# Kernel tuning notes

Measured on AMD Instinct MI355X. Metric: run time of the kernel, lower is better.

The kernel has to match this reference:

```python
import jax, jax.numpy as jnp
import numpy as np

B, L, D = 8, 1024, 768
H, W, Dd = 16, 16, 4          # token grid, H*W*Dd == L
N, R, K = 16, 48, 4           # d_state, dt_rank, d_conv
EPS = 1e-5


def _physical_pos_embed(batch_params, has_velocity):
    # physical coords [B, L, 3]: (distance, angle, velocity/time)
    h_idx = jnp.arange(H, dtype=jnp.float32)[None, :, None, None]
    w_idx = jnp.arange(W, dtype=jnp.float32)[None, None, :, None]
    d_idx = jnp.arange(Dd, dtype=jnp.float32)[None, None, None, :]
    rres = batch_params[:, 0][:, None, None, None]
    ares = batch_params[:, 1][:, None, None, None]
    vres = batch_params[:, 2][:, None, None, None]
    zero = jnp.zeros((1, H, W, Dd), jnp.float32)
    dist = h_idx * rres + zero
    ang = (w_idx - W / 2) * ares + zero
    vel = jnp.where(has_velocity[:, None, None, None],
                    (d_idx - Dd / 2) * vres, d_idx * vres) + zero
    coords = jnp.stack([dist, ang, vel], axis=-1).reshape(B, L, 3)
    mx = coords.max(axis=1, keepdims=True)
    mn = coords.min(axis=1, keepdims=True)
    rng = mx - mn
    rng = jnp.where(rng > 0, rng, jnp.ones_like(rng))
    coords = (coords - mn) / rng
    # sincos embed: D/3 = 256 dims per coord (even -> pure sin/cos)
    fdim = D // 3
    omega = jnp.arange(fdim // 2, dtype=jnp.float32) / (fdim / 2.0)
    omega = 1.0 / (10000.0 ** omega)                      # [128]
    out = jnp.einsum('blc,f->blcf', coords, omega)        # [B,L,3,128]
    emb = jnp.concatenate([jnp.sin(out), jnp.cos(out)], axis=-1)  # [B,L,3,256]
    return emb.reshape(B, L, D)


def _rmsnorm(x, w):
    return x * jax.lax.rsqrt(jnp.mean(x * x, axis=-1, keepdims=True) + EPS) * w


def _mamba(h, in_proj_w, in_proj_b, conv_w, conv_b, x_proj_w,
           dt_proj_w, dt_proj_b, A_log, D_param, out_proj_w, out_proj_b):
    xz = h @ in_proj_w.T + in_proj_b                      # [B,L,2D]
    x_in, z = xz[..., :D], xz[..., D:]
    # causal depthwise conv1d, kernel K
    xp = jnp.pad(x_in, ((0, 0), (K - 1, 0), (0, 0)))
    x_conv = sum(xp[:, k:k + L, :] * conv_w[:, 0, k] for k in range(K))
    x_conv = jax.nn.silu(x_conv + conv_b)
    x_dbl = x_conv @ x_proj_w.T                           # [B,L,R+2N]
    dt, Bm, Cm = x_dbl[..., :R], x_dbl[..., R:R + N], x_dbl[..., R + N:]
    dt = jax.nn.softplus(dt @ dt_proj_w.T + dt_proj_b)    # [B,L,D]
    A = -jnp.exp(A_log)                                   # [D,N]
    dA = jnp.exp(dt[..., None] * A)                       # [B,L,D,N]
    dBx = dt[..., None] * Bm[:, :, None, :] * x_conv[..., None]

    def step(hst, inp):
        dA_t, dBx_t, C_t = inp
        hst = dA_t * hst + dBx_t                          # [B,D,N]
        y_t = jnp.einsum('bdn,bn->bd', hst, C_t)
        return hst, y_t

    h0 = jnp.zeros((B, D, N), x_in.dtype)
    _, ys = jax.lax.scan(step, h0, (dA.transpose(1, 0, 2, 3),
                                    dBx.transpose(1, 0, 2, 3),
                                    Cm.transpose(1, 0, 2)))
    y = ys.transpose(1, 0, 2) + D_param * x_conv          # [B,L,D]
    y = y * jax.nn.silu(z)
    return y @ out_proj_w.T + out_proj_b


def reference(x, batch_params, has_velocity, norm_w, in_proj_w, in_proj_b,
              conv_w, conv_b, x_proj_w, dt_proj_w, dt_proj_b, A_log,
              D_param, out_proj_w, out_proj_b):
    pos = _physical_pos_embed(batch_params, has_velocity)
    residual = x + pos                                    # ARBlock residual
    hidden = _rmsnorm(residual, norm_w)
    hidden = _mamba(hidden, in_proj_w, in_proj_b, conv_w, conv_b, x_proj_w,
                    dt_proj_w, dt_proj_b, A_log, D_param,
                    out_proj_w, out_proj_b)
    return hidden + residual


def setup_inputs():
    key = jax.random.key(0)
    ks = jax.random.split(key, 12)
    s = 0.02
    return {
        'x': jax.random.normal(ks[0], (B, L, D), jnp.float32),
        'batch_params': jax.random.uniform(ks[1], (B, 4), jnp.float32, 0.01, 1.0),
        'has_velocity': jax.random.randint(ks[2], (B,), 0, 2) > 0,
        'norm_w': jnp.ones((D,), jnp.float32),
        'in_proj_w': jax.random.normal(ks[3], (2 * D, D), jnp.float32) * s,
        'in_proj_b': jnp.zeros((2 * D,), jnp.float32),
        'conv_w': jax.random.normal(ks[4], (D, 1, K), jnp.float32) * 0.3,
        'conv_b': jnp.zeros((D,), jnp.float32),
        'x_proj_w': jax.random.normal(ks[5], (R + 2 * N, D), jnp.float32) * s,
        'dt_proj_w': jax.random.normal(ks[6], (D, R), jnp.float32) * s,
        'dt_proj_b': jax.random.normal(ks[7], (D,), jnp.float32) * 0.1,
        'A_log': jnp.log(jax.random.uniform(ks[8], (D, N), jnp.float32, 1.0, 16.0)),
        'D_param': jnp.ones((D,), jnp.float32),
        'out_proj_w': jax.random.normal(ks[9], (D, D), jnp.float32) * s,
        'out_proj_b': jnp.zeros((D,), jnp.float32),
    }
```

## Files before the change

kernel.cpp:

```cpp
#include <hip/hip_runtime.h>
#include <math.h>

#define BB 8
#define LL 1024
#define DD 768
#define NNs 16
#define RR 48

typedef __attribute__((ext_vector_type(8))) short bf16x8;
typedef __attribute__((ext_vector_type(4))) float f32x4;

__device__ __forceinline__ float silu_f(float v) { return v / (1.0f + __expf(-v)); }

__device__ __forceinline__ short f2bf(float f) {
    union { float f; unsigned u; } v; v.f = f;
    unsigned r = (v.u + 0x7fffu + ((v.u >> 16) & 1u)) >> 16;
    return (short)r;
}

__device__ __forceinline__ void async16(const void* g, void* l) {
    __builtin_amdgcn_global_load_lds((const __attribute__((address_space(1))) void*)g,
                                     (__attribute__((address_space(3))) void*)l,
                                     16, 0, 0);
}

__global__ __launch_bounds__(256) void k_cvt(const float* __restrict__ src,
                                             short* __restrict__ dst, int n4) {
    int i = blockIdx.x * 256 + threadIdx.x;
    if (i < n4) {
        float4 v = ((const float4*)src)[i];
        short4 o = { f2bf(v.x), f2bf(v.y), f2bf(v.z), f2bf(v.w) };
        ((short4*)dst)[i] = o;
    }
}

__global__ __launch_bounds__(256) void k_pos_rms(const float* __restrict__ x,
                                                 const float* __restrict__ norm_w,
                                                 float* __restrict__ res,
                                                 short* __restrict__ hidb) {
    int row = blockIdx.x;
    int l = row & (LL - 1);
    int d3 = l & 3;
    int w = (l >> 2) & 15;
    int h = l >> 6;
    float coord[3] = { h * (1.0f / 15.0f), w * (1.0f / 15.0f), d3 * (1.0f / 3.0f) };
    const float LOG1E4 = 9.210340371976184f;
    int t = threadIdx.x;
    float r[3];
    float s = 0.0f;
#pragma unroll
    for (int i = 0; i < 3; i++) {
        int j = t + i * 256;
        int c = j >> 8;
        int fp = j & 255;
        int f = fp & 127;
        float omega = __expf(-(f * (1.0f / 128.0f)) * LOG1E4);
        float arg = coord[c] * omega;
        float pv = (fp < 128) ? __sinf(arg) : __cosf(arg);
        float rv = x[(size_t)row * DD + j] + pv;
        r[i] = rv;
        s += rv * rv;
    }
#pragma unroll
    for (int off = 32; off; off >>= 1) s += __shfl_xor(s, off, 64);
    __shared__ float ls[4];
    if ((t & 63) == 0) ls[t >> 6] = s;
    __syncthreads();
    s = ls[0] + ls[1] + ls[2] + ls[3];
    float rs = rsqrtf(s * (1.0f / DD) + 1e-5f);
#pragma unroll
    for (int i = 0; i < 3; i++) {
        int j = t + i * 256;
        res[(size_t)row * DD + j] = r[i];
        hidb[(size_t)row * DD + j] = f2bf(r[i] * rs * norm_w[j]);
    }
}

template <int EPI, bool AF32>
__global__ __launch_bounds__(256) void gemm_mfma(const void* __restrict__ Ap,
                                                 const short* __restrict__ Bw,
                                                 int Kd,
                                                 const float* __restrict__ bias,
                                                 const float* __restrict__ resid,
                                                 float* __restrict__ C0,
                                                 float* __restrict__ C1) {
    __shared__ short As[4096];
    __shared__ short Bs[4096];
    int m0 = blockIdx.y * 128;
    int n0 = blockIdx.x * 128;
    int tid = threadIdx.x;
    int lane = tid & 63, wave = tid >> 6;
    int q = lane >> 4, r = lane & 15;
    int wm = wave >> 1, wn = wave & 1;

    const size_t Kb = (size_t)Kd * 2;
    const char* gB0 = (const char*)Bw + (size_t)(n0 + wave * 16 + r) * Kb + q * 16;
    const char* gB1 = gB0 + 64 * Kb;
    char* lB0 = (char*)Bs + wave * 1024;
    char* lB1 = lB0 + 4096;
    const char* gA0 = nullptr; const char* gA1 = nullptr;
    char* lA0 = nullptr; char* lA1 = nullptr;
    if (!AF32) {
        gA0 = (const char*)Ap + (size_t)(m0 + wave * 16 + r) * Kb + q * 16;
        gA1 = gA0 + 64 * Kb;
        lA0 = (char*)As + wave * 1024;
        lA1 = lA0 + 4096;
    }

    f32x4 acc[4][4] = {};

    for (int k0 = 0; k0 < Kd; k0 += 32) {
        if (AF32) {
            const float* Af = (const float*)Ap;
#pragma unroll
            for (int p = 0; p < 2; p++) {
                int m = m0 + (p * 4 + wave) * 16 + r;
                const float* src = Af + (size_t)m * Kd + k0 + q * 8;
                float4 v0 = *(const float4*)src;
                float4 v1 = *(const float4*)(src + 4);
                bf16x8 pk;
                pk[0] = f2bf(v0.x); pk[1] = f2bf(v0.y);
                pk[2] = f2bf(v0.z); pk[3] = f2bf(v0.w);
                pk[4] = f2bf(v1.x); pk[5] = f2bf(v1.y);
                pk[6] = f2bf(v1.z); pk[7] = f2bf(v1.w);
                *(bf16x8*)&As[p * 2048 + wave * 512 + lane * 8] = pk;
            }
        } else {
            async16(gA0, lA0); async16(gA1, lA1);
            gA0 += 64; gA1 += 64;
        }
        async16(gB0, lB0); async16(gB1, lB1);
        gB0 += 64; gB1 += 64;
        __syncthreads();
        bf16x8 af[4], bf[4];
#pragma unroll
        for (int a = 0; a < 4; a++)
            af[a] = *(const bf16x8*)&As[((wm * 4 + a) * 64 + q * 16 + r) * 8];
#pragma unroll
        for (int b = 0; b < 4; b++)
            bf[b] = *(const bf16x8*)&Bs[((wn * 4 + b) * 64 + q * 16 + r) * 8];
#pragma unroll
        for (int a = 0; a < 4; a++)
#pragma unroll
            for (int b = 0; b < 4; b++)
                acc[a][b] = __builtin_amdgcn_mfma_f32_16x16x32_bf16(
                    af[a], bf[b], acc[a][b], 0, 0, 0);
        __syncthreads();
    }

#pragma unroll
    for (int a = 0; a < 4; a++) {
        int mrow = m0 + (wm * 4 + a) * 16 + q * 4;
#pragma unroll
        for (int b = 0; b < 4; b++) {
            int ncol = n0 + (wn * 4 + b) * 16 + r;
            float bb = bias[ncol];
            if (EPI == 1) {
                float* dst = (ncol < DD) ? (C0 + (size_t)mrow * DD + ncol)
                                         : (C1 + (size_t)mrow * DD + (ncol - DD));
#pragma unroll
                for (int e = 0; e < 4; e++)
                    dst[(size_t)e * DD] = acc[a][b][e] + bb;
            } else {
#pragma unroll
                for (int e = 0; e < 4; e++) {
                    size_t idx = (size_t)(mrow + e) * DD + ncol;
                    C0[idx] = acc[a][b][e] + bb + resid[idx];
                }
            }
        }
    }
}

template <int MODE>
__global__ __launch_bounds__(256) void gemm_nt(const float* __restrict__ A, int lda,
                                               const float* __restrict__ Bw, int ldb,
                                               int N, int Kd,
                                               const float* __restrict__ bias,
                                               float* __restrict__ C0, int ldc) {
    __shared__ __align__(16) float As[16][68];
    __shared__ __align__(16) float Bs[16][68];
    int m0 = blockIdx.y * 64;
    int n0 = blockIdx.x * 64;
    int t = threadIdx.x;
    int tx = t & 15, ty = t >> 4;
    int ar = t >> 2;
    int ak = (t & 3) * 4;
    float acc[4][4] = {};
    for (int k0 = 0; k0 < Kd; k0 += 16) {
        float4 av = *(const float4*)(A + (size_t)(m0 + ar) * lda + k0 + ak);
        int brow = n0 + ar;
        if (brow >= N) brow = N - 1;
        float4 bv = *(const float4*)(Bw + (size_t)brow * ldb + k0 + ak);
        As[ak + 0][ar] = av.x; As[ak + 1][ar] = av.y;
        As[ak + 2][ar] = av.z; As[ak + 3][ar] = av.w;
        Bs[ak + 0][ar] = bv.x; Bs[ak + 1][ar] = bv.y;
        Bs[ak + 2][ar] = bv.z; Bs[ak + 3][ar] = bv.w;
        __syncthreads();
#pragma unroll
        for (int kk = 0; kk < 16; kk++) {
            float4 a4 = *(const float4*)&As[kk][ty * 4];
            float4 b4 = *(const float4*)&Bs[kk][tx * 4];
            float aa[4] = { a4.x, a4.y, a4.z, a4.w };
            float bb[4] = { b4.x, b4.y, b4.z, b4.w };
#pragma unroll
            for (int i = 0; i < 4; i++)
#pragma unroll
                for (int j = 0; j < 4; j++) acc[i][j] += aa[i] * bb[j];
        }
        __syncthreads();
    }
    if (MODE == 0) {
#pragma unroll
        for (int i = 0; i < 4; i++) {
            int m = m0 + ty * 4 + i;
#pragma unroll
            for (int j = 0; j < 4; j++) {
                int n = n0 + tx * 4 + j;
                if (n < N) C0[(size_t)m * ldc + n] = acc[i][j];
            }
        }
    } else {
        float4 bi = *(const float4*)(bias + n0 + tx * 4);
        float bl[4] = { bi.x, bi.y, bi.z, bi.w };
#pragma unroll
        for (int i = 0; i < 4; i++) {
            int m = m0 + ty * 4 + i;
            float v[4];
#pragma unroll
            for (int j = 0; j < 4; j++) {
                float u = acc[i][j] + bl[j];
                v[j] = (u > 20.0f) ? u : log1pf(__expf(u));
            }
            float4 o = { v[0], v[1], v[2], v[3] };
            *(float4*)(C0 + (size_t)m * DD + n0 + tx * 4) = o;
        }
    }
}

__global__ __launch_bounds__(256) void k_conv(const float* __restrict__ xin,
                                              const float* __restrict__ cw,
                                              const float* __restrict__ cb,
                                              float* __restrict__ xc) {
    size_t gid = (size_t)blockIdx.x * 256 + threadIdx.x;
    int d = (int)(gid % DD);
    int bt = (int)(gid / DD);
    int tt = bt & (LL - 1);
    float4 w = ((const float4*)cw)[d];
    const float* p = xin + (size_t)bt * DD + d;
    float acc = cb[d];
    if (tt >= 3) acc += p[-3 * DD] * w.x;
    if (tt >= 2) acc += p[-2 * DD] * w.y;
    if (tt >= 1) acc += p[-1 * DD] * w.z;
    acc += p[0] * w.w;
    xc[gid] = silu_f(acc);
}

__global__ __launch_bounds__(256) void k_scan(const float* __restrict__ dtf,
                                              const float* __restrict__ xc,
                                              const float* __restrict__ xdbl,
                                              const float* __restrict__ A_log,
                                              const float* __restrict__ Dp,
                                              float* __restrict__ zy) {
    __shared__ float Pl[32 * 8 * 16];
    __shared__ float Sl[32 * 8 * 16];
    int bid = blockIdx.x;
    int xcd = bid & 7;
    int v = bid >> 3;
    int dtile = xcd * 12 + (v % 12);
    int b = v / 12;
    int d0 = dtile * 8;
    int tid = threadIdx.x;
    int dl = tid & 7;
    int c = tid >> 3;
    int d = d0 + dl;

    float Ac[16];
    {
        const float4* al = (const float4*)(A_log + d * NNs);
#pragma unroll
        for (int i = 0; i < 4; i++) {
            float4 v4 = al[i];
            Ac[i * 4 + 0] = -__expf(v4.x); Ac[i * 4 + 1] = -__expf(v4.y);
            Ac[i * 4 + 2] = -__expf(v4.z); Ac[i * 4 + 3] = -__expf(v4.w);
        }
    }
    size_t rb = ((size_t)(b * LL + c * 32)) * DD + d;
    const float* dtp = dtf + rb;
    const float* xcp = xc + rb;
    float* zp = zy + rb;
    const float* xrow = xdbl + ((size_t)(b * LL + c * 32)) * 80 + RR;

    float P[16], S[16];
#pragma unroll
    for (int n = 0; n < 16; n++) { P[n] = 1.0f; S[n] = 0.0f; }
    for (int i = 0; i < 32; i++) {
        float dtv = dtp[(size_t)i * DD];
        float xcv = xcp[(size_t)i * DD];
        float dx = dtv * xcv;
        const float* Br = xrow + i * 80;
#pragma unroll
        for (int qq = 0; qq < 4; qq++) {
            float4 B4 = *(const float4*)(Br + qq * 4);
            float bl[4] = { B4.x, B4.y, B4.z, B4.w };
#pragma unroll
            for (int j = 0; j < 4; j++) {
                int n = qq * 4 + j;
                float e = __expf(dtv * Ac[n]);
                P[n] *= e;
                S[n] = e * S[n] + dx * bl[j];
            }
        }
    }
    {
        float* pw = &Pl[(c * 8 + dl) * 16];
        float* sw = &Sl[(c * 8 + dl) * 16];
#pragma unroll
        for (int qq = 0; qq < 4; qq++) {
            float4 pv = { P[qq * 4], P[qq * 4 + 1], P[qq * 4 + 2], P[qq * 4 + 3] };
            float4 sv = { S[qq * 4], S[qq * 4 + 1], S[qq * 4 + 2], S[qq * 4 + 3] };
            *(float4*)(pw + qq * 4) = pv;
            *(float4*)(sw + qq * 4) = sv;
        }
    }
    __syncthreads();
    if (tid < 128) {
        int d2 = tid >> 4, n2 = tid & 15;
        float hh = 0.0f;
#pragma unroll
        for (int cc = 0; cc < 32; cc++) {
            int idx = (cc * 8 + d2) * 16 + n2;
            float Pv = Pl[idx], Sv = Sl[idx];
            Pl[idx] = hh;
            hh = Pv * hh + Sv;
        }
    }
    __syncthreads();
    float h[16];
    {
        const float* hr = &Pl[(c * 8 + dl) * 16];
#pragma unroll
        for (int qq = 0; qq < 4; qq++) {
            float4 v4 = *(const float4*)(hr + qq * 4);
            h[qq * 4] = v4.x; h[qq * 4 + 1] = v4.y;
            h[qq * 4 + 2] = v4.z; h[qq * 4 + 3] = v4.w;
        }
    }
    float Dv = Dp[d];
    for (int i = 0; i < 32; i++) {
        float dtv = dtp[(size_t)i * DD];
        float xcv = xcp[(size_t)i * DD];
        float zv  = zp[(size_t)i * DD];
        float dx = dtv * xcv;
        float y = Dv * xcv;
        const float* Br = xrow + i * 80;
#pragma unroll
        for (int qq = 0; qq < 4; qq++) {
            float4 B4 = *(const float4*)(Br + qq * 4);
            float4 C4 = *(const float4*)(Br + 16 + qq * 4);
            float bl[4] = { B4.x, B4.y, B4.z, B4.w };
            float cl[4] = { C4.x, C4.y, C4.z, C4.w };
#pragma unroll
            for (int j = 0; j < 4; j++) {
                int n = qq * 4 + j;
                float e = __expf(dtv * Ac[n]);
                h[n] = e * h[n] + dx * bl[j];
                y += h[n] * cl[j];
            }
        }
        zp[(size_t)i * DD] = y * silu_f(zv);
    }
}

extern "C" void kernel_launch(void* const* d_in, const int* in_sizes, int n_in,
                              void* d_out, int out_size, void* d_ws, size_t ws_size,
                              hipStream_t stream) {
    const float* x      = (const float*)d_in[0];
    const float* norm_w = (const float*)d_in[3];
    const float* in_w   = (const float*)d_in[4];
    const float* in_b   = (const float*)d_in[5];
    const float* conv_w = (const float*)d_in[6];
    const float* conv_b = (const float*)d_in[7];
    const float* xp_w   = (const float*)d_in[8];
    const float* dt_w   = (const float*)d_in[9];
    const float* dt_b   = (const float*)d_in[10];
    const float* A_log  = (const float*)d_in[11];
    const float* Dp     = (const float*)d_in[12];
    const float* out_w  = (const float*)d_in[13];
    const float* out_b  = (const float*)d_in[14];
    float* out = (float*)d_out;

    const size_t S = (size_t)BB * LL * DD;
    float* res   = (float*)d_ws;
    float* slotA = res + S;
    float* slotB = slotA + S;
    float* zf    = slotB + S;
    float* xdbl  = zf + S;
    short* inw_b  = (short*)(xdbl + (size_t)BB * LL * 80);
    short* outw_b = inw_b + 1536 * DD;

    short* hidb = (short*)slotA;
    float* xc   = slotA;
    float* xin  = slotB;
    float* dtf  = slotB;

    const int M = BB * LL;

    k_cvt<<<(1536 * DD / 4 + 255) / 256, 256, 0, stream>>>(in_w, inw_b, 1536 * DD / 4);
    k_cvt<<<(DD * DD / 4 + 255) / 256, 256, 0, stream>>>(out_w, outw_b, DD * DD / 4);

    k_pos_rms<<<M, 256, 0, stream>>>(x, norm_w, res, hidb);

    gemm_mfma<1, false><<<dim3(1536 / 128, M / 128), 256, 0, stream>>>(
        hidb, inw_b, DD, in_b, nullptr, xin, zf);

    k_conv<<<(int)(S / 256), 256, 0, stream>>>(xin, conv_w, conv_b, xc);

    gemm_nt<0><<<dim3(2, M / 64), 256, 0, stream>>>(
        xc, DD, xp_w, DD, RR + 2 * NNs, DD, nullptr, xdbl, 80);

    gemm_nt<2><<<dim3(DD / 64, M / 64), 256, 0, stream>>>(
        xdbl, 80, dt_w, RR, DD, RR, dt_b, dtf, DD);

    k_scan<<<768, 256, 0, stream>>>(dtf, xc, xdbl, A_log, Dp, zf);

    gemm_mfma<3, true><<<dim3(DD / 128, M / 128), 256, 0, stream>>>(
        zf, outw_b, DD, out_b, res, out, nullptr);
}
```

Baseline: 381.0 us.

## Store conv output and dt in channel-major layout for contiguous scan loads

The conv kernel now tiles through shared memory and writes xc transposed as [B,D,L]. The x_proj GEMM reads that transposed layout and the dt GEMM writes dt transposed, so the scan can load 4 consecutive timesteps per thread as one vector instead of strided single loads. The scan also switches to a raw v_exp_f32 (exp2 with A prescaled by log2e), prefetches the next group of dt/xc/z values, and sets launch bounds to 3 blocks. The cost is extra LDS traffic in conv and transposed-store patterns in the GEMMs.

```diff
diff --git a/kernel.cpp b/kernel.cpp
--- a/kernel.cpp
+++ b/kernel.cpp
@@ -16,6 +16,12 @@
     union { float f; unsigned u; } v; v.f = f;
     unsigned r = (v.u + 0x7fffu + ((v.u >> 16) & 1u)) >> 16;
     return (short)r;
+}
+
+__device__ __forceinline__ float exp2_fast(float x) {
+    float r;
+    asm("v_exp_f32 %0, %1" : "=v"(r) : "v"(x));
+    return r;
 }
 
 __device__ __forceinline__ void async16(const void* g, void* l) {
@@ -186,14 +192,23 @@
     int tx = t & 15, ty = t >> 4;
     int ar = t >> 2;
     int ak = (t & 3) * 4;
+    int bA = m0 >> 10;
+    int t0A = m0 & 1023;
     float acc[4][4] = {};
     for (int k0 = 0; k0 < Kd; k0 += 16) {
-        float4 av = *(const float4*)(A + (size_t)(m0 + ar) * lda + k0 + ak);
+        if (MODE == 0) {
+            int kr = t >> 4;
+            int am = (t & 15) * 4;
+            float4 av = *(const float4*)&A[((size_t)(bA * DD) + k0 + kr) * LL + t0A + am];
+            *(float4*)&As[kr][am] = av;
+        } else {
+            float4 av = *(const float4*)(A + (size_t)(m0 + ar) * lda + k0 + ak);
+            As[ak + 0][ar] = av.x; As[ak + 1][ar] = av.y;
+            As[ak + 2][ar] = av.z; As[ak + 3][ar] = av.w;
+        }
         int brow = n0 + ar;
         if (brow >= N) brow = N - 1;
         float4 bv = *(const float4*)(Bw + (size_t)brow * ldb + k0 + ak);
-        As[ak + 0][ar] = av.x; As[ak + 1][ar] = av.y;
-        As[ak + 2][ar] = av.z; As[ak + 3][ar] = av.w;
         Bs[ak + 0][ar] = bv.x; Bs[ak + 1][ar] = bv.y;
         Bs[ak + 2][ar] = bv.z; Bs[ak + 3][ar] = bv.w;
         __syncthreads();
@@ -223,17 +238,20 @@
     } else {
         float4 bi = *(const float4*)(bias + n0 + tx * 4);
         float bl[4] = { bi.x, bi.y, bi.z, bi.w };
-#pragma unroll
-        for (int i = 0; i < 4; i++) {
-            int m = m0 + ty * 4 + i;
-            float v[4];
+        float vv[4][4];
+#pragma unroll
+        for (int i = 0; i < 4; i++)
 #pragma unroll
             for (int j = 0; j < 4; j++) {
                 float u = acc[i][j] + bl[j];
-                v[j] = (u > 20.0f) ? u : log1pf(__expf(u));
+                vv[i][j] = (u > 20.0f) ? u : log1pf(__expf(u));
             }
-            float4 o = { v[0], v[1], v[2], v[3] };
-            *(float4*)(C0 + (size_t)m * DD + n0 + tx * 4) = o;
+        int tt0 = t0A + ty * 4;
+#pragma unroll
+        for (int j = 0; j < 4; j++) {
+            int dcol = n0 + tx * 4 + j;
+            float4 o = { vv[0][j], vv[1][j], vv[2][j], vv[3][j] };
+            *(float4*)(C0 + ((size_t)(bA * DD) + dcol) * LL + tt0) = o;
         }
     }
 }
@@ -241,27 +259,51 @@
 __global__ __launch_bounds__(256) void k_conv(const float* __restrict__ xin,
                                               const float* __restrict__ cw,
                                               const float* __restrict__ cb,
-                                              float* __restrict__ xc) {
-    size_t gid = (size_t)blockIdx.x * 256 + threadIdx.x;
-    int d = (int)(gid % DD);
-    int bt = (int)(gid / DD);
-    int tt = bt & (LL - 1);
+                                              float* __restrict__ xcT) {
+    __shared__ float xs[67][65];
+    int d0 = blockIdx.x * 64;
+    int t0 = blockIdx.y * 64;
+    int b  = blockIdx.z;
+    int tid = threadIdx.x;
+    for (int idx = tid; idx < 67 * 16; idx += 256) {
+        int row = idx >> 4, c4 = (idx & 15) * 4;
+        int t = t0 - 3 + row;
+        float4 v = { 0.f, 0.f, 0.f, 0.f };
+        if (t >= 0) v = *(const float4*)&xin[((size_t)(b * LL + t)) * DD + d0 + c4];
+        xs[row][c4 + 0] = v.x; xs[row][c4 + 1] = v.y;
+        xs[row][c4 + 2] = v.z; xs[row][c4 + 3] = v.w;
+    }
+    __syncthreads();
+    int dl = tid >> 2;
+    int ts = (tid & 3) * 16;
+    int d = d0 + dl;
     float4 w = ((const float4*)cw)[d];
-    const float* p = xin + (size_t)bt * DD + d;
-    float acc = cb[d];
-    if (tt >= 3) acc += p[-3 * DD] * w.x;
-    if (tt >= 2) acc += p[-2 * DD] * w.y;
-    if (tt >= 1) acc += p[-1 * DD] * w.z;
-    acc += p[0] * w.w;
-    xc[gid] = silu_f(acc);
-}
-
-__global__ __launch_bounds__(256) void k_scan(const float* __restrict__ dtf,
-                                              const float* __restrict__ xc,
-                                              const float* __restrict__ xdbl,
-                                              const float* __restrict__ A_log,
-                                              const float* __restrict__ Dp,
-                                              float* __restrict__ zy) {
+    float bias = cb[d];
+    float x0 = xs[ts + 0][dl], x1 = xs[ts + 1][dl], x2 = xs[ts + 2][dl];
+    float* outp = xcT + ((size_t)(b * DD + d)) * LL + t0 + ts;
+    float o0, o1, o2, o3;
+#pragma unroll
+    for (int i = 0; i < 16; i++) {
+        float x3 = xs[ts + i + 3][dl];
+        float a = silu_f(bias + x0 * w.x + x1 * w.y + x2 * w.z + x3 * w.w);
+        if ((i & 3) == 0) o0 = a;
+        else if ((i & 3) == 1) o1 = a;
+        else if ((i & 3) == 2) o2 = a;
+        else {
+            o3 = a;
+            float4 o = { o0, o1, o2, o3 };
+            *(float4*)(outp + i - 3) = o;
+        }
+        x0 = x1; x1 = x2; x2 = x3;
+    }
+}
+
+__global__ __launch_bounds__(256, 3) void k_scan(const float* __restrict__ dtT,
+                                                 const float* __restrict__ xcT,
+                                                 const float* __restrict__ xdbl,
+                                                 const float* __restrict__ A_log,
+                                                 const float* __restrict__ Dp,
+                                                 float* __restrict__ zy) {
     __shared__ float Pl[32 * 8 * 16];
     __shared__ float Sl[32 * 8 * 16];
     int bid = blockIdx.x;
@@ -275,41 +317,55 @@
     int c = tid >> 3;
     int d = d0 + dl;
 
+    const float LOG2E = 1.4426950408889634f;
     float Ac[16];
     {
         const float4* al = (const float4*)(A_log + d * NNs);
 #pragma unroll
         for (int i = 0; i < 4; i++) {
             float4 v4 = al[i];
-            Ac[i * 4 + 0] = -__expf(v4.x); Ac[i * 4 + 1] = -__expf(v4.y);
-            Ac[i * 4 + 2] = -__expf(v4.z); Ac[i * 4 + 3] = -__expf(v4.w);
-        }
-    }
+            Ac[i * 4 + 0] = -__expf(v4.x) * LOG2E;
+            Ac[i * 4 + 1] = -__expf(v4.y) * LOG2E;
+            Ac[i * 4 + 2] = -__expf(v4.z) * LOG2E;
+            Ac[i * 4 + 3] = -__expf(v4.w) * LOG2E;
+        }
+    }
+    size_t tb = ((size_t)(b * DD + d)) * LL + c * 32;
+    const float* dtp = dtT + tb;
+    const float* xcp = xcT + tb;
     size_t rb = ((size_t)(b * LL + c * 32)) * DD + d;
-    const float* dtp = dtf + rb;
-    const float* xcp = xc + rb;
     float* zp = zy + rb;
     const float* xrow = xdbl + ((size_t)(b * LL + c * 32)) * 80 + RR;
 
     float P[16], S[16];
 #pragma unroll
     for (int n = 0; n < 16; n++) { P[n] = 1.0f; S[n] = 0.0f; }
-    for (int i = 0; i < 32; i++) {
-        float dtv = dtp[(size_t)i * DD];
-        float xcv = xcp[(size_t)i * DD];
-        float dx = dtv * xcv;
-        const float* Br = xrow + i * 80;
-#pragma unroll
-        for (int qq = 0; qq < 4; qq++) {
-            float4 B4 = *(const float4*)(Br + qq * 4);
-            float bl[4] = { B4.x, B4.y, B4.z, B4.w };
-#pragma unroll
-            for (int j = 0; j < 4; j++) {
-                int n = qq * 4 + j;
-                float e = __expf(dtv * Ac[n]);
-                P[n] *= e;
-                S[n] = e * S[n] + dx * bl[j];
+    {
+        f32x4 dtA = *(const f32x4*)dtp;
+        f32x4 xcA = *(const f32x4*)xcp;
+        for (int g = 0; g < 8; g++) {
+            int off = (g < 7) ? (g * 4 + 4) : (g * 4);
+            f32x4 dtN = *(const f32x4*)(dtp + off);
+            f32x4 xcN = *(const f32x4*)(xcp + off);
+#pragma unroll
+            for (int u = 0; u < 4; u++) {
+                float dtv = dtA[u], xcv = xcA[u];
+                float dx = dtv * xcv;
+                const float* Br = xrow + (g * 4 + u) * 80;
+#pragma unroll
+                for (int qq = 0; qq < 4; qq++) {
+                    float4 B4 = *(const float4*)(Br + qq * 4);
+                    float bl[4] = { B4.x, B4.y, B4.z, B4.w };
+#pragma unroll
+                    for (int j = 0; j < 4; j++) {
+                        int n = qq * 4 + j;
+                        float e = exp2_fast(dtv * Ac[n]);
+                        P[n] *= e;
+                        S[n] = e * S[n] + dx * bl[j];
+                    }
+                }
             }
+            dtA = dtN; xcA = xcN;
         }
     }
     {
@@ -347,28 +403,45 @@
         }
     }
     float Dv = Dp[d];
-    for (int i = 0; i < 32; i++) {
-        float dtv = dtp[(size_t)i * DD];
-        float xcv = xcp[(size_t)i * DD];
-        float zv  = zp[(size_t)i * DD];
-        float dx = dtv * xcv;
-        float y = Dv * xcv;
-        const float* Br = xrow + i * 80;
-#pragma unroll
-        for (int qq = 0; qq < 4; qq++) {
-            float4 B4 = *(const float4*)(Br + qq * 4);
-            float4 C4 = *(const float4*)(Br + 16 + qq * 4);
-            float bl[4] = { B4.x, B4.y, B4.z, B4.w };
-            float cl[4] = { C4.x, C4.y, C4.z, C4.w };
-#pragma unroll
-            for (int j = 0; j < 4; j++) {
-                int n = qq * 4 + j;
-                float e = __expf(dtv * Ac[n]);
-                h[n] = e * h[n] + dx * bl[j];
-                y += h[n] * cl[j];
+    {
+        f32x4 dtA = *(const f32x4*)dtp;
+        f32x4 xcA = *(const f32x4*)xcp;
+        float zA0 = zp[0], zA1 = zp[DD], zA2 = zp[2 * DD], zA3 = zp[3 * DD];
+        for (int g = 0; g < 8; g++) {
+            int off = (g < 7) ? (g * 4 + 4) : (g * 4);
+            f32x4 dtN = *(const f32x4*)(dtp + off);
+            f32x4 xcN = *(const f32x4*)(xcp + off);
+            float zN0 = zp[(size_t)(off + 0) * DD];
+            float zN1 = zp[(size_t)(off + 1) * DD];
+            float zN2 = zp[(size_t)(off + 2) * DD];
+            float zN3 = zp[(size_t)(off + 3) * DD];
+#pragma unroll
+            for (int u = 0; u < 4; u++) {
+                int i = g * 4 + u;
+                float dtv = dtA[u], xcv = xcA[u];
+                float zv = (u == 0) ? zA0 : (u == 1) ? zA1 : (u == 2) ? zA2 : zA3;
+                float dx = dtv * xcv;
+                float y = Dv * xcv;
+                const float* Br = xrow + i * 80;
+#pragma unroll
+                for (int qq = 0; qq < 4; qq++) {
+                    float4 B4 = *(const float4*)(Br + qq * 4);
+                    float4 C4 = *(const float4*)(Br + 16 + qq * 4);
+                    float bl[4] = { B4.x, B4.y, B4.z, B4.w };
+                    float cl[4] = { C4.x, C4.y, C4.z, C4.w };
+#pragma unroll
+                    for (int j = 0; j < 4; j++) {
+                        int n = qq * 4 + j;
+                        float e = exp2_fast(dtv * Ac[n]);
+                        h[n] = e * h[n] + dx * bl[j];
+                        y += h[n] * cl[j];
+                    }
+                }
+                zp[(size_t)i * DD] = y * silu_f(zv);
             }
-        }
-        zp[(size_t)i * DD] = y * silu_f(zv);
+            dtA = dtN; xcA = xcN;
+            zA0 = zN0; zA1 = zN1; zA2 = zN2; zA3 = zN3;
+        }
     }
 }
 
@@ -400,9 +473,9 @@
     short* outw_b = inw_b + 1536 * DD;
 
     short* hidb = (short*)slotA;
-    float* xc   = slotA;
+    float* xcT  = slotA;
     float* xin  = slotB;
-    float* dtf  = slotB;
+    float* dtT  = slotB;
 
     const int M = BB * LL;
 
@@ -414,15 +487,15 @@
     gemm_mfma<1, false><<<dim3(1536 / 128, M / 128), 256, 0, stream>>>(
         hidb, inw_b, DD, in_b, nullptr, xin, zf);
 
-    k_conv<<<(int)(S / 256), 256, 0, stream>>>(xin, conv_w, conv_b, xc);
+    k_conv<<<dim3(DD / 64, LL / 64, BB), 256, 0, stream>>>(xin, conv_w, conv_b, xcT);
 
     gemm_nt<0><<<dim3(2, M / 64), 256, 0, stream>>>(
-        xc, DD, xp_w, DD, RR + 2 * NNs, DD, nullptr, xdbl, 80);
+        xcT, DD, xp_w, DD, RR + 2 * NNs, DD, nullptr, xdbl, 80);
 
     gemm_nt<2><<<dim3(DD / 64, M / 64), 256, 0, stream>>>(
-        xdbl, 80, dt_w, RR, DD, RR, dt_b, dtf, DD);
-
-    k_scan<<<768, 256, 0, stream>>>(dtf, xc, xdbl, A_log, Dp, zf);
+        xdbl, 80, dt_w, RR, DD, RR, dt_b, dtT, DD);
+
+    k_scan<<<768, 256, 0, stream>>>(dtT, xcT, xdbl, A_log, Dp, zf);
 
     gemm_mfma<3, true><<<dim3(DD / 128, M / 128), 256, 0, stream>>>(
         zf, outw_b, DD, out_b, res, out, nullptr);
```

New measurement: 413.4 us. 8.5% more time.
